# Kernel optimization log

Measured on AMD Instinct MI355X. Metric: run time of the kernel, lower is better.

Reference implementation:

```python
import jax, jax.numpy as jnp
import numpy as np

H = 128
EPS = 1e-5
INFERENCE_BIAS = 0.1


def setup_inputs() -> dict:
    key = jax.random.key(0)
    ks = jax.random.split(key, 10)
    n_users, n_foods, E = 100000, 50000, 1000000
    z_user = jax.random.normal(ks[0], (n_users, H), dtype=jnp.float32)
    z_food = jax.random.normal(ks[1], (n_foods, H), dtype=jnp.float32)
    row = jax.random.randint(ks[2], (E,), 0, n_users, dtype=jnp.int64)
    col = jax.random.randint(ks[3], (E,), 0, n_foods, dtype=jnp.int64)
    # lin1: Linear(2H -> H); lin2: Linear(H -> 1)
    W1 = jax.random.normal(ks[4], (H, 2 * H), dtype=jnp.float32) * (1.0 / np.sqrt(2 * H))
    b1 = jnp.zeros((H,), dtype=jnp.float32)
    gamma = jnp.ones((H,), dtype=jnp.float32)
    beta = jnp.zeros((H,), dtype=jnp.float32)
    running_mean = jax.random.normal(ks[5], (H,), dtype=jnp.float32) * 0.1
    running_var = jnp.abs(jax.random.normal(ks[6], (H,), dtype=jnp.float32)) * 0.1 + 1.0
    W2 = jax.random.normal(ks[7], (1, H), dtype=jnp.float32) * (1.0 / np.sqrt(H))
    b2 = jnp.zeros((1,), dtype=jnp.float32)
    return {"z_user": z_user, "z_food": z_food, "row": row, "col": col,
            "W1": W1, "b1": b1, "gamma": gamma, "beta": beta,
            "running_mean": running_mean, "running_var": running_var,
            "W2": W2, "b2": b2}


def reference(z_user, z_food, row, col, W1, b1, gamma, beta,
              running_mean, running_var, W2, b2):
    # gather per-edge endpoint embeddings and concat: [E, 2H]
    z = jnp.concatenate([z_user[row], z_food[col]], axis=-1)
    h = z @ W1.T + b1                                        # [E, H]
    # BatchNorm1d in eval mode: running statistics
    h = (h - running_mean) * jax.lax.rsqrt(running_var + EPS) * gamma + beta
    h = jax.nn.relu(h)                                        # dropout is identity in eval
    out = h @ W2.T + b2                                       # [E, 1]
    return jax.nn.sigmoid((out + INFERENCE_BIAS).reshape(-1)) # [E]
```

## Files before the change

### kernel.cpp

```cpp
#include <hip/hip_runtime.h>
#include <hip/hip_bf16.h>
#include <math.h>

#define H 128
#define EPS 1e-5f
#define INF_BIAS 0.1f

#define BIN_SHIFT 10
#define CAP 24576
#define NBMAX 64

typedef __attribute__((ext_vector_type(8))) short bf16x8;
typedef __attribute__((ext_vector_type(4))) float f32x4;
typedef __attribute__((ext_vector_type(4))) unsigned int u32x4;

__device__ inline unsigned short f2bf_rne(float f) {
    unsigned u = __float_as_uint(f);
    u += 0x7fffu + ((u >> 16) & 1u);
    return (unsigned short)(u >> 16);
}
__device__ inline float bf2f(unsigned short h) {
    return __uint_as_float(((unsigned)h) << 16);
}
__device__ inline unsigned pack2(float a, float b) {
    return (unsigned)f2bf_rne(a) | ((unsigned)f2bf_rne(b) << 16);
}
__device__ inline float2 unpack2(unsigned v) {
    float2 r;
    r.x = __uint_as_float(v << 16);
    r.y = __uint_as_float(v & 0xffff0000u);
    return r;
}

__global__ void prep_kernel(
    const float* __restrict__ W1, const float* __restrict__ b1,
    const float* __restrict__ gamma, const float* __restrict__ beta,
    const float* __restrict__ rm, const float* __restrict__ rv,
    unsigned short* __restrict__ Wswz_u, unsigned short* __restrict__ Wswz_f,
    float* __restrict__ d_user, int* __restrict__ binCursor, int useBinned)
{
    const int f    = blockIdx.x;
    const int half = f >> 4, nt = (f >> 2) & 3, kt = f & 3;
    const int t    = threadIdx.x;
    const int c    = t & 15, q = t >> 4;

    if (useBinned && f == 0) binCursor[t] = 0;

    const int j  = half * 64 + (c >> 2) * 16 + nt * 4 + (c & 3);
    const float a = gamma[j] * rsqrtf(rv[j] + EPS);
    const int k0 = kt * 32 + q * 8;

    unsigned short wu[8], wf[8];
    #pragma unroll
    for (int i = 0; i < 8; ++i) {
        wu[i] = f2bf_rne(a * W1[(size_t)j * (2 * H) + k0 + i]);
        wf[i] = f2bf_rne(a * W1[(size_t)j * (2 * H) + H + k0 + i]);
    }
    const size_t dst = (size_t)f * 512 + (size_t)t * 8;
    #pragma unroll
    for (int i = 0; i < 8; ++i) { Wswz_u[dst + i] = wu[i]; Wswz_f[dst + i] = wf[i]; }

    if (kt == 0 && q == 0) d_user[j] = a * (b1[j] - rm[j]) + beta[j];
}

__global__ __launch_bounds__(256, 2) void proj_mfma(
    const float* __restrict__ z_user, const float* __restrict__ z_food,
    const unsigned short* __restrict__ Wswz_u, const unsigned short* __restrict__ Wswz_f,
    const float* __restrict__ d_user,
    unsigned short* __restrict__ U, unsigned short* __restrict__ F,
    int n_users, int n_foods, int GU, int GB)
{
    const bool userMode = (blockIdx.x < (unsigned)GU);
    const float* Z;
    const unsigned short* Wsrc;
    unsigned short* Out;
    int n, blk0, nblk;
    if (userMode) { Z = z_user; Wsrc = Wswz_u; Out = U; n = n_users; blk0 = blockIdx.x;      nblk = GU; }
    else          { Z = z_food; Wsrc = Wswz_f; Out = F; n = n_foods; blk0 = blockIdx.x - GU; nblk = GB - GU; }
    const int tiles = n >> 4;

    const int wave = threadIdx.x >> 6;
    const int lane = threadIdx.x & 63;
    const int c = lane & 15;
    const int q = lane >> 4;
    const int wg   = blk0 * 4 + wave;
    const int half = wg & 1;
    const int pair = wg >> 1;
    const int stride = nblk * 2;

    bf16x8 wf[4][4];
    #pragma unroll
    for (int nt = 0; nt < 4; ++nt)
        #pragma unroll
        for (int kt = 0; kt < 4; ++kt)
            wf[nt][kt] = *(const bf16x8*)(Wsrc + (size_t)(half * 16 + nt * 4 + kt) * 512 + lane * 8);

    f32x4 dvec[4];
    #pragma unroll
    for (int nt = 0; nt < 4; ++nt) {
        if (userMode) {
            float4 d = *(const float4*)(d_user + half * 64 + q * 16 + nt * 4);
            dvec[nt] = (f32x4){d.x, d.y, d.z, d.w};
        } else {
            dvec[nt] = (f32x4){0.f, 0.f, 0.f, 0.f};
        }
    }

    auto loadZ = [&](int t, float4 zb[8]) {
        const float* zrow = Z + (size_t)(min(t, tiles - 1) * 16 + c) * H;
        #pragma unroll
        for (int kt = 0; kt < 4; ++kt) {
            const int k0 = kt * 32 + q * 8;
            zb[2 * kt + 0] = ((const float4*)(zrow + k0))[0];
            zb[2 * kt + 1] = ((const float4*)(zrow + k0))[1];
        }
    };

    auto computeStore = [&](int t, const float4 zb[8]) {
        f32x4 acc[4];
        #pragma unroll
        for (int nt = 0; nt < 4; ++nt) acc[nt] = dvec[nt];

        #pragma unroll
        for (int kt = 0; kt < 4; ++kt) {
            float4 za = zb[2 * kt + 0];
            float4 zv = zb[2 * kt + 1];
            bf16x8 zhi, zlo;
            {
                float v[8] = {za.x, za.y, za.z, za.w, zv.x, zv.y, zv.z, zv.w};
                #pragma unroll
                for (int i = 0; i < 8; ++i) {
                    unsigned short hi = f2bf_rne(v[i]);
                    unsigned short lo = f2bf_rne(v[i] - bf2f(hi));
                    zhi[i] = (short)hi; zlo[i] = (short)lo;
                }
            }
            #pragma unroll
            for (int nt = 0; nt < 4; ++nt) {
                acc[nt] = __builtin_amdgcn_mfma_f32_16x16x32_bf16(wf[nt][kt], zhi, acc[nt], 0, 0, 0);
                acc[nt] = __builtin_amdgcn_mfma_f32_16x16x32_bf16(wf[nt][kt], zlo, acc[nt], 0, 0, 0);
            }
        }

        if (t < tiles) {
            const int r = t * 16 + c;
            unsigned short* obase = Out + (size_t)r * H + half * 64 + q * 16;
            uint4 p0, p1;
            p0.x = pack2(acc[0][0], acc[0][1]); p0.y = pack2(acc[0][2], acc[0][3]);
            p0.z = pack2(acc[1][0], acc[1][1]); p0.w = pack2(acc[1][2], acc[1][3]);
            p1.x = pack2(acc[2][0], acc[2][1]); p1.y = pack2(acc[2][2], acc[2][3]);
            p1.z = pack2(acc[3][0], acc[3][1]); p1.w = pack2(acc[3][2], acc[3][3]);
            *(uint4*)(obase)     = p0;
            *(uint4*)(obase + 8) = p1;
        }
    };

    int nIt = (tiles + stride - 1) / stride;
    nIt = (nIt + 1) & ~1;

    float4 zb0[8], zb1[8];
    int t = pair;
    loadZ(t, zb0);
    for (int it = 0; it < nIt; it += 2) {
        loadZ(t + stride, zb1);
        computeStore(t, zb0);
        if (it + 2 < nIt) loadZ(t + 2 * stride, zb0);
        computeStore(t + stride, zb1);
        t += 2 * stride;
    }
}

__global__ __launch_bounds__(256) void bin_scatter(
    const int* __restrict__ row, const int* __restrict__ col, int E,
    int* __restrict__ binCursor,
    int* __restrict__ bpk, int* __restrict__ slotOf)
{
    __shared__ int h[NBMAX];
    __shared__ int cur[NBMAX];
    const int t = threadIdx.x;
    const int chunk = (E + gridDim.x - 1) / gridDim.x;
    const int e0 = blockIdx.x * chunk;
    const int e1 = min(E, e0 + chunk);

    if (t < NBMAX) h[t] = 0;
    __syncthreads();
    for (int e = e0 + t; e < e1; e += 256)
        atomicAdd(&h[col[e] >> BIN_SHIFT], 1);
    __syncthreads();
    if (t < NBMAX) {
        const int c_ = h[t];
        const int old = c_ ? atomicAdd(&binCursor[t], c_) : 0;
        cur[t] = t * CAP + old;
    }
    __syncthreads();
    for (int e = e0 + t; e < e1; e += 256) {
        const int c = col[e];
        const int b = c >> BIN_SHIFT;
        int pos = atomicAdd(&cur[b], 1);
        pos = min(pos, (b + 1) * CAP - 1);
        bpk[pos]   = (row[e] << BIN_SHIFT) | (c & ((1 << BIN_SHIFT) - 1));
        slotOf[e]  = pos;
    }
}

__global__ __launch_bounds__(256) void edge_binned(
    const unsigned short* __restrict__ U, const unsigned short* __restrict__ F,
    const int* __restrict__ bpk, const int* __restrict__ binCursor,
    const float* __restrict__ W2, const float* __restrict__ b2,
    float* __restrict__ res)
{
    const int lane  = threadIdx.x & 15;
    const int g     = (blockIdx.x * blockDim.x + threadIdx.x) >> 4;
    const int slot0 = g * 4;
    const int bin   = slot0 / CAP;
    const int cnt   = min(binCursor[bin], CAP);
    const int idx0  = slot0 - bin * CAP;
    if (idx0 >= cnt) return;

    const float4 w2a = ((const float4*)W2)[2 * lane];
    const float4 w2b = ((const float4*)W2)[2 * lane + 1];
    const float bias = b2[0] + INF_BIAS;
    const int   fbase = bin << BIN_SHIFT;

    int iu[4], ifo[4];
    #pragma unroll
    for (int i = 0; i < 4; ++i) {
        const int s = (idx0 + i < cnt) ? (slot0 + i) : slot0;
        const int v = bpk[s];
        iu[i]  = v >> BIN_SHIFT;
        ifo[i] = fbase + (v & ((1 << BIN_SHIFT) - 1));
    }
    u32x4 uv[4];
    uint4 fv[4];
    #pragma unroll
    for (int i = 0; i < 4; ++i) {
        uv[i] = __builtin_nontemporal_load(((const u32x4*)(U + (size_t)iu[i] * H)) + lane);
        fv[i] = ((const uint4*)(F + (size_t)ifo[i] * H))[lane];
    }
    float r[4];
    #pragma unroll
    for (int i = 0; i < 4; ++i) {
        float2 u0 = unpack2(uv[i][0]), f0 = unpack2(fv[i].x);
        float2 u1 = unpack2(uv[i][1]), f1 = unpack2(fv[i].y);
        float2 u2 = unpack2(uv[i][2]), f2 = unpack2(fv[i].z);
        float2 u3 = unpack2(uv[i][3]), f3 = unpack2(fv[i].w);

        float s =
            w2a.x * fmaxf(u0.x + f0.x, 0.0f) +
            w2a.y * fmaxf(u0.y + f0.y, 0.0f) +
            w2a.z * fmaxf(u1.x + f1.x, 0.0f) +
            w2a.w * fmaxf(u1.y + f1.y, 0.0f) +
            w2b.x * fmaxf(u2.x + f2.x, 0.0f) +
            w2b.y * fmaxf(u2.y + f2.y, 0.0f) +
            w2b.z * fmaxf(u3.x + f3.x, 0.0f) +
            w2b.w * fmaxf(u3.y + f3.y, 0.0f);

        s += __shfl_xor(s, 8, 16);
        s += __shfl_xor(s, 4, 16);
        s += __shfl_xor(s, 2, 16);
        s += __shfl_xor(s, 1, 16);

        const float x = s + bias;
        r[i] = 1.0f / (1.0f + __expf(-x));
    }
    if (lane == 0) {
        float4 o; o.x = r[0]; o.y = r[1]; o.z = r[2]; o.w = r[3];
        *(float4*)(res + slot0) = o;
    }
}

__global__ __launch_bounds__(256) void unscatter(
    const float* __restrict__ res, const int* __restrict__ slotOf,
    float* __restrict__ out, int E)
{
    const int tid = blockIdx.x * blockDim.x + threadIdx.x;
    const int nT  = gridDim.x * blockDim.x;
    const int n4  = E >> 2;
    for (int i = tid; i < n4; i += nT) {
        int4 s = ((const int4*)slotOf)[i];
        float4 o;
        o.x = res[s.x]; o.y = res[s.y]; o.z = res[s.z]; o.w = res[s.w];
        ((float4*)out)[i] = o;
    }
    for (int e = (n4 << 2) + tid; e < E; e += nT)
        out[e] = res[slotOf[e]];
}

#define EUN 4
__global__ __launch_bounds__(256) void edge_kernel(
    const unsigned short* __restrict__ U, const unsigned short* __restrict__ F,
    const int* __restrict__ row, const int* __restrict__ col,
    const float* __restrict__ W2, const float* __restrict__ b2,
    float* __restrict__ out, int E)
{
    const int lane = threadIdx.x & 15;
    const int g  = (blockIdx.x * blockDim.x + threadIdx.x) >> 4;
    const int nG = (gridDim.x * blockDim.x) >> 4;

    const float4 w2a = ((const float4*)W2)[2 * lane];
    const float4 w2b = ((const float4*)W2)[2 * lane + 1];
    const float bias = b2[0] + INF_BIAS;

    for (int e0 = g; e0 < E; e0 += EUN * nG) {
        int iu[EUN], ifo[EUN];
        #pragma unroll
        for (int i = 0; i < EUN; ++i) {
            int e  = e0 + i * nG;
            int ec = (e < E) ? e : e0;
            iu[i]  = row[ec];
            ifo[i] = col[ec];
        }
        uint4 uv[EUN], fv[EUN];
        #pragma unroll
        for (int i = 0; i < EUN; ++i) {
            uv[i] = ((const uint4*)(U + (size_t)iu[i]  * H))[lane];
            fv[i] = ((const uint4*)(F + (size_t)ifo[i] * H))[lane];
        }
        #pragma unroll
        for (int i = 0; i < EUN; ++i) {
            float2 u0 = unpack2(uv[i].x), f0 = unpack2(fv[i].x);
            float2 u1 = unpack2(uv[i].y), f1 = unpack2(fv[i].y);
            float2 u2 = unpack2(uv[i].z), f2 = unpack2(fv[i].z);
            float2 u3 = unpack2(uv[i].w), f3 = unpack2(fv[i].w);

            float s =
                w2a.x * fmaxf(u0.x + f0.x, 0.0f) +
                w2a.y * fmaxf(u0.y + f0.y, 0.0f) +
                w2a.z * fmaxf(u1.x + f1.x, 0.0f) +
                w2a.w * fmaxf(u1.y + f1.y, 0.0f) +
                w2b.x * fmaxf(u2.x + f2.x, 0.0f) +
                w2b.y * fmaxf(u2.y + f2.y, 0.0f) +
                w2b.z * fmaxf(u3.x + f3.x, 0.0f) +
                w2b.w * fmaxf(u3.y + f3.y, 0.0f);

            s += __shfl_xor(s, 8, 16);
            s += __shfl_xor(s, 4, 16);
            s += __shfl_xor(s, 2, 16);
            s += __shfl_xor(s, 1, 16);

            const int e = e0 + i * nG;
            if (lane == 0 && e < E) {
                float x = s + bias;
                out[e] = 1.0f / (1.0f + __expf(-x));
            }
        }
    }
}

extern "C" void kernel_launch(void* const* d_in, const int* in_sizes, int n_in,
                              void* d_out, int out_size, void* d_ws, size_t ws_size,
                              hipStream_t stream) {
    const float* z_user = (const float*)d_in[0];
    const float* z_food = (const float*)d_in[1];
    const int*   row    = (const int*)d_in[2];
    const int*   col    = (const int*)d_in[3];
    const float* W1     = (const float*)d_in[4];
    const float* b1     = (const float*)d_in[5];
    const float* gamma  = (const float*)d_in[6];
    const float* beta   = (const float*)d_in[7];
    const float* rm     = (const float*)d_in[8];
    const float* rv     = (const float*)d_in[9];
    const float* W2     = (const float*)d_in[10];
    const float* b2     = (const float*)d_in[11];
    float* out = (float*)d_out;

    const int n_users = in_sizes[0] / H;
    const int n_foods = in_sizes[1] / H;
    const int E       = in_sizes[2];

    unsigned short* U      = (unsigned short*)d_ws;
    unsigned short* F      = U + (size_t)n_users * H;
    unsigned short* Wswz_u = F + (size_t)n_foods * H;
    unsigned short* Wswz_f = Wswz_u + H * H;
    float*          d_usr  = (float*)(Wswz_f + H * H);
    int*            binCursor = (int*)(d_usr + H);
    int*            bpk    = binCursor + NBMAX;

    const int nb = (n_foods + (1 << BIN_SHIFT) - 1) >> BIN_SHIFT;
    int*   slotOf = bpk + (size_t)nb * CAP;
    float* res    = (float*)(slotOf + (size_t)E);
    const size_t need = (size_t)((char*)(res + (size_t)nb * CAP) - (char*)d_ws);
    const bool binned = (nb >= 1 && nb <= NBMAX &&
                         n_users <= (1 << (31 - BIN_SHIFT)) &&
                         ws_size >= need);

    prep_kernel<<<32, 64, 0, stream>>>(W1, b1, gamma, beta, rm, rv,
                                       Wswz_u, Wswz_f, d_usr,
                                       binCursor, binned ? 1 : 0);

    if (binned)
        bin_scatter<<<1024, 256, 0, stream>>>(row, col, E, binCursor, bpk, slotOf);

    const int GU = 342, GB = 512;
    proj_mfma<<<GB, 256, 0, stream>>>(z_user, z_food, Wswz_u, Wswz_f, d_usr,
                                      U, F, n_users, n_foods, GU, GB);

    if (binned) {
        edge_binned<<<nb * (CAP / 64), 256, 0, stream>>>(U, F, bpk, binCursor,
                                                         W2, b2, res);
        unscatter<<<2048, 256, 0, stream>>>(res, slotOf, out, E);
    } else {
        edge_kernel<<<8192, 256, 0, stream>>>(U, F, row, col, W2, b2, out, E);
    }
}
```

Before: 228.0 us.

## Stage bin scatter through LDS and swizzle edge block order across XCDs

The bin scatter kernel now processes fixed 1024-edge chunks per block. It computes a local prefix over bins, stages packed values and global positions in LDS, and then writes bpk as one pass, so each bin's writes are contiguous and coalesced instead of scattered one by one. The edge_binned kernel remaps block indices so that consecutive bins are spread across the 8 XCDs, which is meant to improve L2 locality of food embeddings per die. The cost is more LDS use and an extra synchronisation. The remap also assumes gridDim is a multiple of 8; if it is not, some blocks are never covered.

```diff
diff --git a/kernel.cpp b/kernel.cpp
--- a/kernel.cpp
+++ b/kernel.cpp
@@ -9,6 +9,7 @@
 #define BIN_SHIFT 10
 #define CAP 24576
 #define NBMAX 64
+#define BS_CHUNK 1024
 
 typedef __attribute__((ext_vector_type(8))) short bf16x8;
 typedef __attribute__((ext_vector_type(4))) float f32x4;
@@ -176,31 +177,61 @@
     int* __restrict__ bpk, int* __restrict__ slotOf)
 {
     __shared__ int h[NBMAX];
-    __shared__ int cur[NBMAX];
-    const int t = threadIdx.x;
-    const int chunk = (E + gridDim.x - 1) / gridDim.x;
-    const int e0 = blockIdx.x * chunk;
-    const int e1 = min(E, e0 + chunk);
+    __shared__ int pfx[NBMAX];
+    __shared__ int gb[NBMAX];
+    __shared__ int vbuf[BS_CHUNK];
+    __shared__ int gposbuf[BS_CHUNK];
+
+    const int t  = threadIdx.x;
+    const int e0 = blockIdx.x * BS_CHUNK;
+    const int e1 = min(E, e0 + BS_CHUNK);
+    const int nE = e1 - e0;
+    if (nE <= 0) return;
 
     if (t < NBMAX) h[t] = 0;
     __syncthreads();
-    for (int e = e0 + t; e < e1; e += 256)
-        atomicAdd(&h[col[e] >> BIN_SHIFT], 1);
-    __syncthreads();
-    if (t < NBMAX) {
-        const int c_ = h[t];
-        const int old = c_ ? atomicAdd(&binCursor[t], c_) : 0;
-        cur[t] = t * CAP + old;
-    }
-    __syncthreads();
+
+    int rr[4], bb[4], co[4];
+    int myN = 0;
     for (int e = e0 + t; e < e1; e += 256) {
         const int c = col[e];
-        const int b = c >> BIN_SHIFT;
-        int pos = atomicAdd(&cur[b], 1);
-        pos = min(pos, (b + 1) * CAP - 1);
-        bpk[pos]   = (row[e] << BIN_SHIFT) | (c & ((1 << BIN_SHIFT) - 1));
-        slotOf[e]  = pos;
-    }
+        rr[myN] = row[e];
+        bb[myN] = c >> BIN_SHIFT;
+        co[myN] = c & ((1 << BIN_SHIFT) - 1);
+        atomicAdd(&h[bb[myN]], 1);
+        ++myN;
+    }
+    __syncthreads();
+
+    if (t < NBMAX) {
+        const int cnt = h[t];
+        int v = cnt;
+        #pragma unroll
+        for (int ofs = 1; ofs < 64; ofs <<= 1) {
+            int u = __shfl_up(v, ofs, 64);
+            if (t >= ofs) v += u;
+        }
+        pfx[t] = v - cnt;
+        const int old = cnt ? atomicAdd(&binCursor[t], cnt) : 0;
+        gb[t] = t * CAP + old;
+        h[t]  = v - cnt;
+    }
+    __syncthreads();
+
+    #pragma unroll 4
+    for (int i = 0; i < myN; ++i) {
+        const int b    = bb[i];
+        const int lpos = atomicAdd(&h[b], 1);
+        int gp = gb[b] + (lpos - pfx[b]);
+        gp = min(gp, (b + 1) * CAP - 1);
+        vbuf[lpos]    = (rr[i] << BIN_SHIFT) | co[i];
+        gposbuf[lpos] = gp;
+        slotOf[e0 + t + i * 256] = gp;
+    }
+    __syncthreads();
+
+    for (int i = t; i < nE; i += 256)
+        bpk[gposbuf[i]] = vbuf[i];
 }
 
 __global__ __launch_bounds__(256) void edge_binned(
@@ -209,8 +240,10 @@
     const float* __restrict__ W2, const float* __restrict__ b2,
     float* __restrict__ res)
 {
+    const int cpx   = gridDim.x >> 3;
+    const int vb    = (blockIdx.x & 7) * cpx + (blockIdx.x >> 3);
     const int lane  = threadIdx.x & 15;
-    const int g     = (blockIdx.x * blockDim.x + threadIdx.x) >> 4;
+    const int g     = (vb * 256 + (int)threadIdx.x) >> 4;
     const int slot0 = g * 4;
     const int bin   = slot0 / CAP;
     const int cnt   = min(binCursor[bin], CAP);
@@ -389,7 +422,8 @@
                                        binCursor, binned ? 1 : 0);
 
     if (binned)
-        bin_scatter<<<1024, 256, 0, stream>>>(row, col, E, binCursor, bpk, slotOf);
+        bin_scatter<<<(E + BS_CHUNK - 1) / BS_CHUNK, 256, 0, stream>>>(
+            row, col, E, binCursor, bpk, slotOf);
 
     const int GU = 342, GB = 512;
     proj_mfma<<<GB, 256, 0, stream>>>(z_user, z_food, Wswz_u, Wswz_f, d_usr,
```

After: 225.5 us. No clear change (-1.1%).
